# Optimization experiments

Hardware: AMD Instinct MI355X
Metric: run time of the kernel (lower is better)

The kernel has to match this reference:

```python
import jax, jax.numpy as jnp
import numpy as np

B, S, H = 64, 512, 768   # n_blocks, seq_len, hidden
C, M = 50, 2000          # n_characters, n_mentions
T = B * S                # total_seq_len
NEG_INF = -jnp.inf


def setup_inputs() -> dict:
    key = jax.random.key(0)
    ks = jax.random.split(key, 16)
    story_embeddings = jax.random.normal(ks[0], (B, S, H), dtype=jnp.float32)

    # additive log masks: 0.0 = allowed token, -inf = blocked (matches softmax(score + mask))
    names_bin = jax.random.bernoulli(ks[1], 0.05, (C, S)).at[:, 0].set(True)  # every char has >=1 name token
    names_mask = jnp.where(names_bin, 0.0, NEG_INF).astype(jnp.float32)

    utt_bin = jax.random.bernoulli(ks[2], 0.02, (C, T))
    utt_bin = utt_bin.at[40:].set(False)  # chars 40..49 have no utterances -> nan_to_num path
    utterances_mask = jnp.where(utt_bin, 0.0, NEG_INF).astype(jnp.float32)

    men_bin = jax.random.bernoulli(ks[3], 0.01, (M, T)).at[:, 0].set(True)
    mentions_mask = jnp.where(men_bin, 0.0, NEG_INF).astype(jnp.float32)

    mention_character_ids = jax.random.randint(ks[4], (M,), 0, 45, dtype=jnp.int32)  # chars 45..49 mention-less

    def lin(k):
        return 0.02 * jax.random.normal(k, (H,), dtype=jnp.float32)

    return {
        "story_embeddings": story_embeddings,
        "names_mask": names_mask,
        "utterances_mask": utterances_mask,
        "mentions_mask": mentions_mask,
        "mention_character_ids": mention_character_ids,
        "w_name_tok": lin(ks[5]), "b_name_tok": jnp.float32(0.0),
        "w_name": lin(ks[6]), "b_name": jnp.float32(0.0),
        "w_men_tok": lin(ks[7]), "b_men_tok": jnp.float32(0.0),
        "w_men": lin(ks[8]), "b_men": jnp.float32(0.0),
        "w_utt": lin(ks[9]), "b_utt": jnp.float32(0.0),
        "w_comb": lin(ks[10]), "b_comb": jnp.float32(0.0),
    }


def reference(story_embeddings, names_mask, utterances_mask, mentions_mask,
              mention_character_ids, w_name_tok, b_name_tok, w_name, b_name,
              w_men_tok, b_men_tok, w_men, b_men, w_utt, b_utt, w_comb, b_comb):
    n_char = names_mask.shape[0]
    n_blocks, seqlen, hidden = story_embeddings.shape
    se_flat = story_embeddings.reshape(n_blocks * seqlen, hidden)  # [T,H]

    # ---- name representation ----
    nts = story_embeddings @ w_name_tok + b_name_tok                       # [B,S]
    n_attn = jax.nn.softmax(nts[None, :, :] + names_mask[:, None, :], axis=2)  # [C,B,S]
    names_emb = jnp.einsum('cbs,bsh->cbh', n_attn, story_embeddings)       # [C,B,H]
    n_score = names_emb @ w_name + b_name                                  # [C,B]
    name_e = jnp.einsum('cb,cbh->ch', jax.nn.softmax(n_score, axis=1), names_emb)

    # ---- mention representation (segment softmax over mentions per character) ----
    mts = se_flat @ w_men_tok + b_men_tok                                  # [T]
    m_attn = jax.nn.softmax(mentions_mask + mts[None, :], axis=1)          # [M,T]
    m_emb = m_attn @ se_flat                                               # [M,H]
    m_score = m_emb @ w_men + b_men                                        # [M]
    seg = mention_character_ids
    seg_max = jax.ops.segment_max(m_score, seg, num_segments=n_char)       # [C]
    ex = jnp.exp(m_score - seg_max[seg])                                   # [M]
    den = jax.ops.segment_sum(ex, seg, num_segments=n_char)                # [C]
    mw = ex / den[seg]                                                     # [M]
    mention_e = jax.ops.segment_sum(mw[:, None] * m_emb, seg, num_segments=n_char)  # [C,H]; empty chars -> 0

    # ---- utterance representation ----
    uts = se_flat @ w_utt + b_utt                                          # [T]
    u_attn = jnp.nan_to_num(jax.nn.softmax(utterances_mask + uts[None, :], axis=1), nan=0.0)
    utt_e = u_attn @ se_flat                                               # [C,H]

    # ---- combine ----
    emb = jnp.stack([name_e, mention_e, utt_e], axis=1)                    # [C,3,H]
    score = emb @ w_comb + b_comb                                          # [C,3]
    has_mention = jax.ops.segment_sum(jnp.ones_like(m_score), seg, num_segments=n_char) > 0
    has_utt = jnp.any(utterances_mask == 0, axis=1)
    zeros = jnp.zeros((n_char,), dtype=score.dtype)
    mask = jnp.stack([zeros,
                      jnp.where(has_mention, 0.0, NEG_INF := -jnp.inf),
                      jnp.where(has_utt, 0.0, -jnp.inf)], axis=1)          # [C,3]
    attn = jax.nn.softmax(score + mask, axis=1)
    return jnp.einsum('ck,ckh->ch', attn, emb)                             # [C,H]
```

## Files before the change

### kernel.cpp

```cpp
#include <hip/hip_runtime.h>
#include <cmath>

#define Bn 64
#define Sn 512
#define Hn 768
#define Cn 50
#define Mn 2000
#define Tn (Bn*Sn)
#define MCAP 1024
#define NP 128
#define TC 256
#define HT 128

__global__ __launch_bounds__(256) void k_proj(
    const float* __restrict__ se,
    const float* __restrict__ w_ntok, const float* __restrict__ b_ntok,
    const float* __restrict__ w_name,
    const float* __restrict__ w_mtok, const float* __restrict__ b_mtok,
    const float* __restrict__ w_men,
    const float* __restrict__ w_utt, const float* __restrict__ b_utt,
    const float* __restrict__ w_comb,
    float* __restrict__ nts, float* __restrict__ p_name,
    float* __restrict__ mts, float* __restrict__ p_men,
    float* __restrict__ uts, float* __restrict__ p_comb)
{
    int wv = threadIdx.x >> 6, lane = threadIdx.x & 63;
    int gw = blockIdx.x * 4 + wv;
    float4 w[6][3];
    const float4* warr[6] = {(const float4*)w_ntok, (const float4*)w_name,
                             (const float4*)w_mtok, (const float4*)w_men,
                             (const float4*)w_utt,  (const float4*)w_comb};
#pragma unroll
    for (int j = 0; j < 6; j++)
#pragma unroll
        for (int k = 0; k < 3; k++) w[j][k] = warr[j][lane + 64*k];
    float b0 = b_ntok[0], b2 = b_mtok[0], b4 = b_utt[0];
    for (int rr = 0; rr < 8; rr++) {
        int r = gw*8 + rr;
        const float4* se4 = (const float4*)(se + (size_t)r * Hn);
        float s0=0,s1=0,s2=0,s3=0,s4=0,s5=0;
#pragma unroll
        for (int k = 0; k < 3; k++) {
            float4 v = se4[lane + 64*k];
            s0 += v.x*w[0][k].x + v.y*w[0][k].y + v.z*w[0][k].z + v.w*w[0][k].w;
            s1 += v.x*w[1][k].x + v.y*w[1][k].y + v.z*w[1][k].z + v.w*w[1][k].w;
            s2 += v.x*w[2][k].x + v.y*w[2][k].y + v.z*w[2][k].z + v.w*w[2][k].w;
            s3 += v.x*w[3][k].x + v.y*w[3][k].y + v.z*w[3][k].z + v.w*w[3][k].w;
            s4 += v.x*w[4][k].x + v.y*w[4][k].y + v.z*w[4][k].z + v.w*w[4][k].w;
            s5 += v.x*w[5][k].x + v.y*w[5][k].y + v.z*w[5][k].z + v.w*w[5][k].w;
        }
#pragma unroll
        for (int off = 32; off >= 1; off >>= 1) {
            s0 += __shfl_xor(s0, off); s1 += __shfl_xor(s1, off);
            s2 += __shfl_xor(s2, off); s3 += __shfl_xor(s3, off);
            s4 += __shfl_xor(s4, off); s5 += __shfl_xor(s5, off);
        }
        if (lane == 0) {
            nts[r]    = s0 + b0;
            p_name[r] = s1;
            mts[r]    = s2 + b2;
            p_men[r]  = s3;
            uts[r]    = s4 + b4;
            p_comb[r] = s5;
        }
    }
}

__global__ __launch_bounds__(256) void k_scan(
    const float* __restrict__ mmask, const float* __restrict__ mts,
    const float* __restrict__ p_men, const float* __restrict__ p_comb,
    const float* __restrict__ b_men_p,
    const float* __restrict__ umask, const float* __restrict__ uts,
    const float* __restrict__ nm_mask, const float* __restrict__ nts,
    const float* __restrict__ p_name, const float* __restrict__ b_name_p,
    float* __restrict__ m_score, float* __restrict__ mcv, float* __restrict__ denm,
    int* __restrict__ midx, float* __restrict__ mwgt, int* __restrict__ mcnt,
    float* __restrict__ m1u, float* __restrict__ denu, float* __restrict__ sc2,
    float* __restrict__ n_score, float* __restrict__ sc_n,
    float* __restrict__ m1n, float* __restrict__ denn)
{
    int tid = threadIdx.x;
    int wv = tid >> 6, lane = tid & 63;

    __shared__ int scnt;
    __shared__ int   sT[MCAP];
    __shared__ float sV[MCAP];
    __shared__ float sr1[4], sr2[4], sr3[4], sr4[4];

    if (blockIdx.x >= Mn + Cn) {
        int idx = (blockIdx.x - Mn - Cn) * 4 + wv;
        int c = idx >> 6, b = idx & 63;
        float v[8];
        float mx = -INFINITY;
#pragma unroll
        for (int k = 0; k < 8; k++) {
            int s = lane + 64*k;
            float val = nm_mask[c*Sn + s] + nts[b*Sn + s];
            v[k] = val;
            mx = fmaxf(mx, val);
        }
#pragma unroll
        for (int off = 32; off >= 1; off >>= 1) mx = fmaxf(mx, __shfl_xor(mx, off));
        float d = 0, sn = 0, sc = 0;
#pragma unroll
        for (int k = 0; k < 8; k++) {
            int s = lane + 64*k;
            int t = b*Sn + s;
            float e = __expf(v[k] - mx);
            d += e; sn += e * p_name[t]; sc += e * p_comb[t];
        }
#pragma unroll
        for (int off = 32; off >= 1; off >>= 1) {
            d += __shfl_xor(d, off); sn += __shfl_xor(sn, off); sc += __shfl_xor(sc, off);
        }
        if (lane == 0) {
            n_score[idx] = sn / d + b_name_p[0];
            sc_n[idx]    = sc / d;
            m1n[idx]     = mx;
            denn[idx]    = d;
        }
        return;
    }

    bool isU = blockIdx.x >= Mn;
    int row = isU ? (blockIdx.x - Mn) : blockIdx.x;
    if (tid == 0) scnt = 0;
    __syncthreads();

    const float4* row4 = (const float4*)((isU ? umask : mmask) + (size_t)row * Tn);
    const float*  vals = isU ? uts : mts;

    for (int k = 0; k < Tn/4/256; k++) {
        int i = tid + k*256;
        float4 f = row4[i];
        float fm[4] = {f.x, f.y, f.z, f.w};
#pragma unroll
        for (int j = 0; j < 4; j++) {
            bool act = (fm[j] == 0.0f);
            unsigned long long bm = __ballot(act);
            if (bm) {
                int tot = __popcll(bm);
                int pos = __popcll(bm & ((1ull << lane) - 1ull));
                int base;
                if (lane == 0) base = atomicAdd(&scnt, tot);
                base = __builtin_amdgcn_readfirstlane(base);
                int s = base + pos;
                if (act && s < MCAP) sT[s] = i*4 + j;
            }
        }
    }
    __syncthreads();
    int n = (scnt < MCAP) ? scnt : MCAP;

    float mx = -INFINITY;
    for (int i = tid; i < n; i += 256) {
        float v = vals[sT[i]];
        sV[i] = v;
        mx = fmaxf(mx, v);
    }
#pragma unroll
    for (int off = 32; off >= 1; off >>= 1) mx = fmaxf(mx, __shfl_xor(mx, off));
    if (lane == 0) sr1[wv] = mx;
    __syncthreads();
    mx = fmaxf(fmaxf(sr1[0], sr1[1]), fmaxf(sr1[2], sr1[3]));

    float d = 0, nm = 0, nc = 0;
    if (!isU) {
        int* gi = midx + (size_t)row * MCAP;
        float* gwp = mwgt + (size_t)row * MCAP;
        for (int i = tid; i < n; i += 256) {
            float e = __expf(sV[i] - mx);
            int t = sT[i];
            d += e; nm += e * p_men[t]; nc += e * p_comb[t];
            gi[i] = t; gwp[i] = e;
        }
    } else {
        for (int i = tid; i < n; i += 256) {
            float e = __expf(sV[i] - mx);
            d += e; nc += e * p_comb[sT[i]];
        }
    }
#pragma unroll
    for (int off = 32; off >= 1; off >>= 1) {
        d += __shfl_xor(d, off); nm += __shfl_xor(nm, off); nc += __shfl_xor(nc, off);
    }
    if (lane == 0) { sr2[wv] = d; sr3[wv] = nm; sr4[wv] = nc; }
    __syncthreads();
    if (tid == 0) {
        float dd = sr2[0]+sr2[1]+sr2[2]+sr2[3];
        float sm = sr3[0]+sr3[1]+sr3[2]+sr3[3];
        float sc = sr4[0]+sr4[1]+sr4[2]+sr4[3];
        if (!isU) {
            m_score[row] = sm/dd + b_men_p[0];
            mcv[row]     = sc/dd;
            denm[row]    = dd;
            mcnt[row]    = n;
        } else {
            m1u[row]  = mx;
            denu[row] = dd;
            sc2[row]  = (dd > 0.f) ? sc/dd : 0.f;
        }
    }
}

__global__ __launch_bounds__(256) void k_small(
    const float* __restrict__ n_score, const float* __restrict__ sc_n,
    const int* __restrict__ seg, const float* __restrict__ m_score, const float* __restrict__ mcv,
    float* __restrict__ bw, float* __restrict__ sc0,
    float* __restrict__ segmax, float* __restrict__ segden, float* __restrict__ sc1)
{
    int tid = threadIdx.x;
    if (blockIdx.x < Cn) {
        int c = blockIdx.x;
        if (tid < 64) {
            int lane = tid;
            int idx = c*Bn + lane;
            float v = n_score[idx];
            float mx = v;
#pragma unroll
            for (int off = 32; off >= 1; off >>= 1) mx = fmaxf(mx, __shfl_xor(mx, off));
            float e = __expf(v - mx);
            float d = e, s = e * sc_n[idx];
#pragma unroll
            for (int off = 32; off >= 1; off >>= 1) { d += __shfl_xor(d, off); s += __shfl_xor(s, off); }
            bw[idx] = e / d;
            if (lane == 0) sc0[c] = s / d;
        }
    } else {
        int c = blockIdx.x - Cn;
        float mx = -INFINITY;
        for (int m = tid; m < Mn; m += 256)
            if (seg[m] == c) mx = fmaxf(mx, m_score[m]);
        __shared__ float sm[256];
        sm[tid] = mx; __syncthreads();
        for (int s = 128; s > 0; s >>= 1) { if (tid < s) sm[tid] = fmaxf(sm[tid], sm[tid+s]); __syncthreads(); }
        mx = sm[0];
        float d = 0, s1 = 0;
        if (mx != -INFINITY) {
            for (int m = tid; m < Mn; m += 256)
                if (seg[m] == c) { float e = __expf(m_score[m] - mx); d += e; s1 += e * mcv[m]; }
        }
        __shared__ float sd[256], ss[256];
        sd[tid] = d; ss[tid] = s1; __syncthreads();
        for (int s = 128; s > 0; s >>= 1) { if (tid < s) { sd[tid] += sd[tid+s]; ss[tid] += ss[tid+s]; } __syncthreads(); }
        if (tid == 0) {
            segmax[c] = mx;
            segden[c] = sd[0];
            sc1[c]    = (sd[0] > 0.f) ? ss[0]/sd[0] : 0.f;
        }
    }
}

__device__ inline void combine_attn(float sc0v, float sc1v, float sc2v,
                                    float sdn, float dnu, float bc,
                                    float& a0, float& a1, float& a2)
{
    float s0 = sc0v + bc;
    bool hasm = sdn > 0.f, hasu = dnu > 0.f;
    float s1 = hasm ? sc1v + bc : -INFINITY;
    float s2 = hasu ? sc2v + bc : -INFINITY;
    float mx = fmaxf(s0, fmaxf(s1, s2));
    float e0 = __expf(s0 - mx);
    float e1 = hasm ? __expf(s1 - mx) : 0.f;
    float e2 = hasu ? __expf(s2 - mx) : 0.f;
    float dd = e0 + e1 + e2;
    a0 = e0/dd; a1 = e1/dd; a2 = e2/dd;
}

__global__ __launch_bounds__(256) void k_buildW(
    const float* __restrict__ nm_mask, const float* __restrict__ nts,
    const float* __restrict__ m1n, const float* __restrict__ denn,
    const float* __restrict__ bw,
    const float* __restrict__ umask, const float* __restrict__ uts,
    const float* __restrict__ m1u, const float* __restrict__ denu,
    const float* __restrict__ sc0, const float* __restrict__ sc1, const float* __restrict__ sc2,
    const float* __restrict__ segden, const float* __restrict__ b_comb_p,
    float* __restrict__ W)
{
    int c = blockIdx.y;
    float a0, a1, a2;
    combine_attn(sc0[c], sc1[c], sc2[c], segden[c], denu[c], b_comb_p[0], a0, a1, a2);
    int t0 = (blockIdx.x * 256 + threadIdx.x) * 4;
    int b = t0 >> 9;
    float4 um = *(const float4*)(umask + (size_t)c * Tn + t0);
    float cn = a0 * bw[c*Bn + b] / denn[c*Bn + b];
    float m1nc = m1n[c*Bn + b];
    float du = denu[c];
    float cu = (du > 0.f) ? a2 / du : 0.f;
    float m1uc = m1u[c];
    float umj[4] = {um.x, um.y, um.z, um.w};
    float rj[4];
#pragma unroll
    for (int j = 0; j < 4; j++) {
        int t = t0 + j;
        int s = t & (Sn-1);
        float w = 0.f;
        if (nm_mask[c*Sn + s] == 0.f) w += cn * __expf(nts[t] - m1nc);
        if (umj[j] == 0.f)            w += cu * __expf(uts[t] - m1uc);
        rj[j] = w;
    }
    *(float4*)(W + (size_t)c * Tn + t0) = make_float4(rj[0], rj[1], rj[2], rj[3]);
}

__global__ __launch_bounds__(64) void k_scatter_men(
    const int* __restrict__ midx, const float* __restrict__ mwgt, const int* __restrict__ mcnt,
    const int* __restrict__ seg,
    const float* __restrict__ m_score, const float* __restrict__ denm,
    const float* __restrict__ segmax, const float* __restrict__ segden,
    const float* __restrict__ sc0, const float* __restrict__ sc1, const float* __restrict__ sc2,
    const float* __restrict__ denu, const float* __restrict__ b_comb_p,
    float* __restrict__ W)
{
    int m = blockIdx.x, tid = threadIdx.x;
    int c = seg[m];
    float a0, a1, a2;
    combine_attn(sc0[c], sc1[c], sc2[c], segden[c], denu[c], b_comb_p[0], a0, a1, a2);
    float coef = a1 * __expf(m_score[m] - segmax[c]) / segden[c] / denm[m];
    int n = mcnt[m];
    const int* gi = midx + (size_t)m * MCAP;
    const float* gwp = mwgt + (size_t)m * MCAP;
    float* Wc = W + (size_t)c * Tn;
    for (int i = tid; i < n; i += 64)
        atomicAdd(&Wc[gi[i]], coef * gwp[i]);
}

#define FMA4(A, WS, V) { A.x += (WS)*(V).x; A.y += (WS)*(V).y; A.z += (WS)*(V).z; A.w += (WS)*(V).w; }
__global__ __launch_bounds__(256) void k_out1(
    const float* __restrict__ W, const float* __restrict__ se, float* __restrict__ partial)
{
    int p = blockIdx.x;
    int h0 = blockIdx.y * HT;
    int tid = threadIdx.x;
    int x = tid & 31, y = tid >> 5;
    __shared__ float sW[56][64];
    __shared__ float sS[64][128];
    float4 acc[7];
#pragma unroll
    for (int i = 0; i < 7; i++) acc[i] = make_float4(0,0,0,0);
    for (int sub = 0; sub < 4; sub++) {
        int tbase = p*TC + sub*64;
        for (int i = tid; i < 896; i += 256) {
            int c = i >> 4, f = i & 15;
            float4 v = (c < Cn) ? *(const float4*)(W + (size_t)c * Tn + tbase + f*4)
                                : make_float4(0,0,0,0);
            *(float4*)&sW[c][f*4] = v;
        }
#pragma unroll
        for (int q = 0; q < 8; q++) {
            int idx = tid + q*256;
            int row = idx >> 5, col = idx & 31;
            *(float4*)&sS[row][col*4] =
                *(const float4*)(se + (size_t)(tbase + row) * Hn + h0 + col*4);
        }
        __syncthreads();
        for (int t4 = 0; t4 < 64; t4 += 4) {
            float4 wq[7];
#pragma unroll
            for (int cc = 0; cc < 7; cc++)
                wq[cc] = *(const float4*)&sW[y*7 + cc][t4];
            float4 v0 = *(const float4*)&sS[t4+0][x*4];
            float4 v1 = *(const float4*)&sS[t4+1][x*4];
            float4 v2 = *(const float4*)&sS[t4+2][x*4];
            float4 v3 = *(const float4*)&sS[t4+3][x*4];
#pragma unroll
            for (int cc = 0; cc < 7; cc++) {
                FMA4(acc[cc], wq[cc].x, v0);
                FMA4(acc[cc], wq[cc].y, v1);
                FMA4(acc[cc], wq[cc].z, v2);
                FMA4(acc[cc], wq[cc].w, v3);
            }
        }
        __syncthreads();
    }
#pragma unroll
    for (int cc = 0; cc < 7; cc++) {
        int c = y*7 + cc;
        if (c < Cn)
            *(float4*)(partial + ((size_t)p * Cn + c) * Hn + h0 + x*4) = acc[cc];
    }
}

__global__ __launch_bounds__(256) void k_out2(
    const float* __restrict__ partial, float* __restrict__ out)
{
    int cell = blockIdx.x * 256 + threadIdx.x;
    if (cell < Cn*Hn) {
        float s = 0.f;
#pragma unroll 8
        for (int p = 0; p < NP; p++)
            s += partial[(size_t)p * (Cn*Hn) + cell];
        out[cell] = s;
    }
}

extern "C" void kernel_launch(void* const* d_in, const int* in_sizes, int n_in,
                              void* d_out, int out_size, void* d_ws, size_t ws_size,
                              hipStream_t stream) {
    const float* se      = (const float*)d_in[0];
    const float* nm_mask = (const float*)d_in[1];
    const float* umask   = (const float*)d_in[2];
    const float* mmask   = (const float*)d_in[3];
    const int*   seg     = (const int*)  d_in[4];
    const float* w_ntok  = (const float*)d_in[5];
    const float* b_ntok  = (const float*)d_in[6];
    const float* w_name  = (const float*)d_in[7];
    const float* b_name  = (const float*)d_in[8];
    const float* w_mtok  = (const float*)d_in[9];
    const float* b_mtok  = (const float*)d_in[10];
    const float* w_men   = (const float*)d_in[11];
    const float* b_men   = (const float*)d_in[12];
    const float* w_utt   = (const float*)d_in[13];
    const float* b_utt   = (const float*)d_in[14];
    const float* w_comb  = (const float*)d_in[15];
    const float* b_comb  = (const float*)d_in[16];
    float* out = (float*)d_out;

    float* ws = (float*)d_ws;
    float* partial = ws;
    float* W       = partial + (size_t)NP*Cn*Hn;
    float* nts     = W + (size_t)Cn*Tn;
    float* p_name  = nts + Tn;
    float* mts     = p_name + Tn;
    float* p_men   = mts + Tn;
    float* uts     = p_men + Tn;
    float* p_comb  = uts + Tn;
    float* n_score = p_comb + Tn;
    float* sc_n    = n_score + Cn*Bn;
    float* bw      = sc_n + Cn*Bn;
    float* m1n     = bw + Cn*Bn;
    float* denn    = m1n + Cn*Bn;
    float* m_score = denn + Cn*Bn;
    float* mcv     = m_score + Mn;
    float* denm    = mcv + Mn;
    float* mwgt    = denm + Mn;
    int*   midx    = (int*)(mwgt + (size_t)Mn*MCAP);
    int*   mcnt    = midx + (size_t)Mn*MCAP;
    float* segmax  = (float*)(mcnt + Mn);
    float* segden  = segmax + Cn;
    float* sc0     = segden + Cn;
    float* sc1     = sc0 + Cn;
    float* sc2     = sc1 + Cn;
    float* m1u     = sc2 + Cn;
    float* denu    = m1u + Cn;

    k_proj<<<1024, 256, 0, stream>>>(se, w_ntok, b_ntok, w_name, w_mtok, b_mtok,
                                     w_men, w_utt, b_utt, w_comb,
                                     nts, p_name, mts, p_men, uts, p_comb);

    k_scan<<<Mn + Cn + (Cn*Bn)/4, 256, 0, stream>>>(
        mmask, mts, p_men, p_comb, b_men,
        umask, uts,
        nm_mask, nts, p_name, b_name,
        m_score, mcv, denm, midx, mwgt, mcnt,
        m1u, denu, sc2,
        n_score, sc_n, m1n, denn);

    k_small<<<2*Cn, 256, 0, stream>>>(n_score, sc_n, seg, m_score, mcv,
                                      bw, sc0, segmax, segden, sc1);

    k_buildW<<<dim3(Tn/1024, Cn), 256, 0, stream>>>(nm_mask, nts, m1n, denn, bw,
                                                    umask, uts, m1u, denu,
                                                    sc0, sc1, sc2, segden, b_comb, W);

    k_scatter_men<<<Mn, 64, 0, stream>>>(midx, mwgt, mcnt, seg, m_score, denm,
                                         segmax, segden, sc0, sc1, sc2, denu, b_comb, W);

    k_out1<<<dim3(NP, Hn/HT), 256, 0, stream>>>(W, se, partial);
    k_out2<<<(Cn*Hn + 255)/256, 256, 0, stream>>>(partial, out);
}
```

Before: 188.4 us.

## Overlap mask scanning with projection and scatter utterance weights sparsely

Merges the projection kernel with the mask-index scan into one launch. Projection blocks are interleaved with scan blocks so the memory-bound mask scan no longer waits for the projection to finish. The index lists now go to global memory, and a second kernel computes the softmax weights from them. The utterance contribution to W is moved out of the dense buildW pass, which re-read the 50x32768 utterance mask, and into the sparse atomic scatter kernel. The cost is extra global traffic for the index lists and more atomics on W.

New measurement: 205.7 us. 9.2% more time.

```diff
diff --git a/kernel.cpp b/kernel.cpp
--- a/kernel.cpp
+++ b/kernel.cpp
@@ -11,9 +11,10 @@
 #define NP 128
 #define TC 256
 #define HT 128
-
-__global__ __launch_bounds__(256) void k_proj(
-    const float* __restrict__ se,
+#define NR (Mn + Cn)
+
+__global__ __launch_bounds__(256) void k_A(
+    const float* __restrict__ se, const float* __restrict__ mmask, const float* __restrict__ umask,
     const float* __restrict__ w_ntok, const float* __restrict__ b_ntok,
     const float* __restrict__ w_name,
     const float* __restrict__ w_mtok, const float* __restrict__ b_mtok,
@@ -22,114 +23,68 @@
     const float* __restrict__ w_comb,
     float* __restrict__ nts, float* __restrict__ p_name,
     float* __restrict__ mts, float* __restrict__ p_men,
-    float* __restrict__ uts, float* __restrict__ p_comb)
-{
-    int wv = threadIdx.x >> 6, lane = threadIdx.x & 63;
-    int gw = blockIdx.x * 4 + wv;
-    float4 w[6][3];
-    const float4* warr[6] = {(const float4*)w_ntok, (const float4*)w_name,
-                             (const float4*)w_mtok, (const float4*)w_men,
-                             (const float4*)w_utt,  (const float4*)w_comb};
-#pragma unroll
-    for (int j = 0; j < 6; j++)
-#pragma unroll
-        for (int k = 0; k < 3; k++) w[j][k] = warr[j][lane + 64*k];
-    float b0 = b_ntok[0], b2 = b_mtok[0], b4 = b_utt[0];
-    for (int rr = 0; rr < 8; rr++) {
-        int r = gw*8 + rr;
-        const float4* se4 = (const float4*)(se + (size_t)r * Hn);
-        float s0=0,s1=0,s2=0,s3=0,s4=0,s5=0;
-#pragma unroll
-        for (int k = 0; k < 3; k++) {
-            float4 v = se4[lane + 64*k];
-            s0 += v.x*w[0][k].x + v.y*w[0][k].y + v.z*w[0][k].z + v.w*w[0][k].w;
-            s1 += v.x*w[1][k].x + v.y*w[1][k].y + v.z*w[1][k].z + v.w*w[1][k].w;
-            s2 += v.x*w[2][k].x + v.y*w[2][k].y + v.z*w[2][k].z + v.w*w[2][k].w;
-            s3 += v.x*w[3][k].x + v.y*w[3][k].y + v.z*w[3][k].z + v.w*w[3][k].w;
-            s4 += v.x*w[4][k].x + v.y*w[4][k].y + v.z*w[4][k].z + v.w*w[4][k].w;
-            s5 += v.x*w[5][k].x + v.y*w[5][k].y + v.z*w[5][k].z + v.w*w[5][k].w;
-        }
-#pragma unroll
-        for (int off = 32; off >= 1; off >>= 1) {
-            s0 += __shfl_xor(s0, off); s1 += __shfl_xor(s1, off);
-            s2 += __shfl_xor(s2, off); s3 += __shfl_xor(s3, off);
-            s4 += __shfl_xor(s4, off); s5 += __shfl_xor(s5, off);
-        }
-        if (lane == 0) {
-            nts[r]    = s0 + b0;
-            p_name[r] = s1;
-            mts[r]    = s2 + b2;
-            p_men[r]  = s3;
-            uts[r]    = s4 + b4;
-            p_comb[r] = s5;
-        }
-    }
-}
-
-__global__ __launch_bounds__(256) void k_scan(
-    const float* __restrict__ mmask, const float* __restrict__ mts,
-    const float* __restrict__ p_men, const float* __restrict__ p_comb,
-    const float* __restrict__ b_men_p,
-    const float* __restrict__ umask, const float* __restrict__ uts,
-    const float* __restrict__ nm_mask, const float* __restrict__ nts,
-    const float* __restrict__ p_name, const float* __restrict__ b_name_p,
-    float* __restrict__ m_score, float* __restrict__ mcv, float* __restrict__ denm,
-    int* __restrict__ midx, float* __restrict__ mwgt, int* __restrict__ mcnt,
-    float* __restrict__ m1u, float* __restrict__ denu, float* __restrict__ sc2,
-    float* __restrict__ n_score, float* __restrict__ sc_n,
-    float* __restrict__ m1n, float* __restrict__ denn)
-{
-    int tid = threadIdx.x;
-    int wv = tid >> 6, lane = tid & 63;
-
+    float* __restrict__ uts, float* __restrict__ p_comb,
+    int* __restrict__ midx, int* __restrict__ mcnt,
+    int* __restrict__ uidx, int* __restrict__ ucnt)
+{
+    int bid = blockIdx.x;
+    int tid = threadIdx.x, wv = tid >> 6, lane = tid & 63;
+
+    int cid = -1, pb = -1;
+    if (bid >= 3072)            cid = 2048 + (bid - 3072);
+    else if (bid % 3 == 2)      pb  = bid / 3;
+    else                        cid = (bid / 3) * 2 + (bid % 3);
+
+    if (pb >= 0) {
+        int gw = pb * 4 + wv;
+        float4 w[6][3];
+        const float4* warr[6] = {(const float4*)w_ntok, (const float4*)w_name,
+                                 (const float4*)w_mtok, (const float4*)w_men,
+                                 (const float4*)w_utt,  (const float4*)w_comb};
+#pragma unroll
+        for (int j = 0; j < 6; j++)
+#pragma unroll
+            for (int k = 0; k < 3; k++) w[j][k] = warr[j][lane + 64*k];
+        float b0 = b_ntok[0], b2 = b_mtok[0], b4 = b_utt[0];
+        for (int rr = 0; rr < 8; rr++) {
+            int r = gw*8 + rr;
+            const float4* se4 = (const float4*)(se + (size_t)r * Hn);
+            float s0=0,s1=0,s2=0,s3=0,s4=0,s5=0;
+#pragma unroll
+            for (int k = 0; k < 3; k++) {
+                float4 v = se4[lane + 64*k];
+                s0 += v.x*w[0][k].x + v.y*w[0][k].y + v.z*w[0][k].z + v.w*w[0][k].w;
+                s1 += v.x*w[1][k].x + v.y*w[1][k].y + v.z*w[1][k].z + v.w*w[1][k].w;
+                s2 += v.x*w[2][k].x + v.y*w[2][k].y + v.z*w[2][k].z + v.w*w[2][k].w;
+                s3 += v.x*w[3][k].x + v.y*w[3][k].y + v.z*w[3][k].z + v.w*w[3][k].w;
+                s4 += v.x*w[4][k].x + v.y*w[4][k].y + v.z*w[4][k].z + v.w*w[4][k].w;
+                s5 += v.x*w[5][k].x + v.y*w[5][k].y + v.z*w[5][k].z + v.w*w[5][k].w;
+            }
+#pragma unroll
+            for (int off = 32; off >= 1; off >>= 1) {
+                s0 += __shfl_xor(s0, off); s1 += __shfl_xor(s1, off);
+                s2 += __shfl_xor(s2, off); s3 += __shfl_xor(s3, off);
+                s4 += __shfl_xor(s4, off); s5 += __shfl_xor(s5, off);
+            }
+            if (lane == 0) {
+                nts[r]    = s0 + b0;
+                p_name[r] = s1;
+                mts[r]    = s2 + b2;
+                p_men[r]  = s3;
+                uts[r]    = s4 + b4;
+                p_comb[r] = s5;
+            }
+        }
+        return;
+    }
+
+    bool isU = cid >= Mn;
+    int row = isU ? (cid - Mn) : cid;
+    const float4* row4 = (const float4*)((isU ? umask : mmask) + (size_t)row * Tn);
+    int* list = isU ? (uidx + (size_t)row * MCAP) : (midx + (size_t)row * MCAP);
     __shared__ int scnt;
-    __shared__ int   sT[MCAP];
-    __shared__ float sV[MCAP];
-    __shared__ float sr1[4], sr2[4], sr3[4], sr4[4];
-
-    if (blockIdx.x >= Mn + Cn) {
-        int idx = (blockIdx.x - Mn - Cn) * 4 + wv;
-        int c = idx >> 6, b = idx & 63;
-        float v[8];
-        float mx = -INFINITY;
-#pragma unroll
-        for (int k = 0; k < 8; k++) {
-            int s = lane + 64*k;
-            float val = nm_mask[c*Sn + s] + nts[b*Sn + s];
-            v[k] = val;
-            mx = fmaxf(mx, val);
-        }
-#pragma unroll
-        for (int off = 32; off >= 1; off >>= 1) mx = fmaxf(mx, __shfl_xor(mx, off));
-        float d = 0, sn = 0, sc = 0;
-#pragma unroll
-        for (int k = 0; k < 8; k++) {
-            int s = lane + 64*k;
-            int t = b*Sn + s;
-            float e = __expf(v[k] - mx);
-            d += e; sn += e * p_name[t]; sc += e * p_comb[t];
-        }
-#pragma unroll
-        for (int off = 32; off >= 1; off >>= 1) {
-            d += __shfl_xor(d, off); sn += __shfl_xor(sn, off); sc += __shfl_xor(sc, off);
-        }
-        if (lane == 0) {
-            n_score[idx] = sn / d + b_name_p[0];
-            sc_n[idx]    = sc / d;
-            m1n[idx]     = mx;
-            denn[idx]    = d;
-        }
-        return;
-    }
-
-    bool isU = blockIdx.x >= Mn;
-    int row = isU ? (blockIdx.x - Mn) : blockIdx.x;
     if (tid == 0) scnt = 0;
     __syncthreads();
-
-    const float4* row4 = (const float4*)((isU ? umask : mmask) + (size_t)row * Tn);
-    const float*  vals = isU ? uts : mts;
-
     for (int k = 0; k < Tn/4/256; k++) {
         int i = tid + k*256;
         float4 f = row4[i];
@@ -141,20 +96,85 @@
             if (bm) {
                 int tot = __popcll(bm);
                 int pos = __popcll(bm & ((1ull << lane) - 1ull));
-                int base;
+                int base = 0;
                 if (lane == 0) base = atomicAdd(&scnt, tot);
                 base = __builtin_amdgcn_readfirstlane(base);
                 int s = base + pos;
-                if (act && s < MCAP) sT[s] = i*4 + j;
+                if (act && s < MCAP) list[s] = i*4 + j;
             }
         }
     }
     __syncthreads();
-    int n = (scnt < MCAP) ? scnt : MCAP;
+    if (tid == 0) {
+        int n = (scnt < MCAP) ? scnt : MCAP;
+        if (isU) ucnt[row] = n; else mcnt[row] = n;
+    }
+}
+
+__global__ __launch_bounds__(256) void k_B(
+    const float* __restrict__ mts, const float* __restrict__ uts,
+    const float* __restrict__ p_men, const float* __restrict__ p_comb,
+    const float* __restrict__ p_name,
+    const float* __restrict__ b_men_p, const float* __restrict__ b_name_p,
+    const float* __restrict__ nm_mask, const float* __restrict__ nts,
+    const int* __restrict__ midx, const int* __restrict__ mcnt,
+    const int* __restrict__ uidx, const int* __restrict__ ucnt,
+    float* __restrict__ m_score, float* __restrict__ mcv, float* __restrict__ denm,
+    float* __restrict__ mwgt,
+    float* __restrict__ denu, float* __restrict__ sc2, float* __restrict__ uwgt,
+    float* __restrict__ n_score, float* __restrict__ sc_n,
+    float* __restrict__ m1n, float* __restrict__ denn)
+{
+    int bid = blockIdx.x;
+    int tid = threadIdx.x, wv = tid >> 6, lane = tid & 63;
+
+    if (bid >= NR) {
+        int idx = (bid - NR) * 4 + wv;
+        int c = idx >> 6, b = idx & 63;
+        float v[8];
+        float mx = -INFINITY;
+#pragma unroll
+        for (int k = 0; k < 8; k++) {
+            int s = lane + 64*k;
+            float val = nm_mask[c*Sn + s] + nts[b*Sn + s];
+            v[k] = val;
+            mx = fmaxf(mx, val);
+        }
+#pragma unroll
+        for (int off = 32; off >= 1; off >>= 1) mx = fmaxf(mx, __shfl_xor(mx, off));
+        float d = 0, sn = 0, sc = 0;
+#pragma unroll
+        for (int k = 0; k < 8; k++) {
+            int s = lane + 64*k;
+            int t = b*Sn + s;
+            float e = __expf(v[k] - mx);
+            d += e; sn += e * p_name[t]; sc += e * p_comb[t];
+        }
+#pragma unroll
+        for (int off = 32; off >= 1; off >>= 1) {
+            d += __shfl_xor(d, off); sn += __shfl_xor(sn, off); sc += __shfl_xor(sc, off);
+        }
+        if (lane == 0) {
+            n_score[idx] = sn / d + b_name_p[0];
+            sc_n[idx]    = sc / d;
+            m1n[idx]     = mx;
+            denn[idx]    = d;
+        }
+        return;
+    }
+
+    bool isU = bid >= Mn;
+    int row = isU ? (bid - Mn) : bid;
+    int n = isU ? ucnt[row] : mcnt[row];
+    const int* gi = isU ? (uidx + (size_t)row * MCAP) : (midx + (size_t)row * MCAP);
+    const float* vals = isU ? uts : mts;
+
+    __shared__ float sV[MCAP];
+    __shared__ float sr1[4], sr2[4], sr3[4], sr4[4];
 
     float mx = -INFINITY;
     for (int i = tid; i < n; i += 256) {
-        float v = vals[sT[i]];
+        float v = vals[gi[i]];
         sV[i] = v;
         mx = fmaxf(mx, v);
     }
@@ -165,20 +185,13 @@
     mx = fmaxf(fmaxf(sr1[0], sr1[1]), fmaxf(sr1[2], sr1[3]));
 
     float d = 0, nm = 0, nc = 0;
-    if (!isU) {
-        int* gi = midx + (size_t)row * MCAP;
-        float* gwp = mwgt + (size_t)row * MCAP;
-        for (int i = tid; i < n; i += 256) {
-            float e = __expf(sV[i] - mx);
-            int t = sT[i];
-            d += e; nm += e * p_men[t]; nc += e * p_comb[t];
-            gi[i] = t; gwp[i] = e;
-        }
-    } else {
-        for (int i = tid; i < n; i += 256) {
-            float e = __expf(sV[i] - mx);
-            d += e; nc += e * p_comb[sT[i]];
-        }
+    float* wout = isU ? (uwgt + (size_t)row * MCAP) : (mwgt + (size_t)row * MCAP);
+    for (int i = tid; i < n; i += 256) {
+        float e = __expf(sV[i] - mx);
+        int t = gi[i];
+        d += e; nc += e * p_comb[t];
+        if (!isU) nm += e * p_men[t];
+        wout[i] = e;
     }
 #pragma unroll
     for (int off = 32; off >= 1; off >>= 1) {
@@ -194,9 +207,7 @@
             m_score[row] = sm/dd + b_men_p[0];
             mcv[row]     = sc/dd;
             denm[row]    = dd;
-            mcnt[row]    = n;
         } else {
-            m1u[row]  = mx;
             denu[row] = dd;
             sc2[row]  = (dd > 0.f) ? sc/dd : 0.f;
         }
@@ -271,8 +282,7 @@
     const float* __restrict__ nm_mask, const float* __restrict__ nts,
     const float* __restrict__ m1n, const float* __restrict__ denn,
     const float* __restrict__ bw,
-    const float* __restrict__ umask, const float* __restrict__ uts,
-    const float* __restrict__ m1u, const float* __restrict__ denu,
+    const float* __restrict__ denu,
     const float* __restrict__ sc0, const float* __restrict__ sc1, const float* __restrict__ sc2,
     const float* __restrict__ segden, const float* __restrict__ b_comb_p,
     float* __restrict__ W)
@@ -282,28 +292,21 @@
     combine_attn(sc0[c], sc1[c], sc2[c], segden[c], denu[c], b_comb_p[0], a0, a1, a2);
     int t0 = (blockIdx.x * 256 + threadIdx.x) * 4;
     int b = t0 >> 9;
-    float4 um = *(const float4*)(umask + (size_t)c * Tn + t0);
     float cn = a0 * bw[c*Bn + b] / denn[c*Bn + b];
     float m1nc = m1n[c*Bn + b];
-    float du = denu[c];
-    float cu = (du > 0.f) ? a2 / du : 0.f;
-    float m1uc = m1u[c];
-    float umj[4] = {um.x, um.y, um.z, um.w};
     float rj[4];
 #pragma unroll
     for (int j = 0; j < 4; j++) {
         int t = t0 + j;
         int s = t & (Sn-1);
-        float w = 0.f;
-        if (nm_mask[c*Sn + s] == 0.f) w += cn * __expf(nts[t] - m1nc);
-        if (umj[j] == 0.f)            w += cu * __expf(uts[t] - m1uc);
-        rj[j] = w;
+        rj[j] = (nm_mask[c*Sn + s] == 0.f) ? cn * __expf(nts[t] - m1nc) : 0.f;
     }
     *(float4*)(W + (size_t)c * Tn + t0) = make_float4(rj[0], rj[1], rj[2], rj[3]);
 }
 
-__global__ __launch_bounds__(64) void k_scatter_men(
+__global__ __launch_bounds__(64) void k_scatter(
     const int* __restrict__ midx, const float* __restrict__ mwgt, const int* __restrict__ mcnt,
+    const int* __restrict__ uidx, const float* __restrict__ uwgt, const int* __restrict__ ucnt,
     const int* __restrict__ seg,
     const float* __restrict__ m_score, const float* __restrict__ denm,
     const float* __restrict__ segmax, const float* __restrict__ segden,
@@ -311,17 +314,33 @@
     const float* __restrict__ denu, const float* __restrict__ b_comb_p,
     float* __restrict__ W)
 {
-    int m = blockIdx.x, tid = threadIdx.x;
-    int c = seg[m];
-    float a0, a1, a2;
-    combine_attn(sc0[c], sc1[c], sc2[c], segden[c], denu[c], b_comb_p[0], a0, a1, a2);
-    float coef = a1 * __expf(m_score[m] - segmax[c]) / segden[c] / denm[m];
-    int n = mcnt[m];
-    const int* gi = midx + (size_t)m * MCAP;
-    const float* gwp = mwgt + (size_t)m * MCAP;
-    float* Wc = W + (size_t)c * Tn;
-    for (int i = tid; i < n; i += 64)
-        atomicAdd(&Wc[gi[i]], coef * gwp[i]);
+    int bid = blockIdx.x, tid = threadIdx.x;
+    if (bid < Mn) {
+        int m = bid;
+        int c = seg[m];
+        float a0, a1, a2;
+        combine_attn(sc0[c], sc1[c], sc2[c], segden[c], denu[c], b_comb_p[0], a0, a1, a2);
+        float coef = a1 * __expf(m_score[m] - segmax[c]) / segden[c] / denm[m];
+        int n = mcnt[m];
+        const int* gi = midx + (size_t)m * MCAP;
+        const float* gwp = mwgt + (size_t)m * MCAP;
+        float* Wc = W + (size_t)c * Tn;
+        for (int i = tid; i < n; i += 64)
+            atomicAdd(&Wc[gi[i]], coef * gwp[i]);
+    } else {
+        int c = bid - Mn;
+        float dn = denu[c];
+        if (dn <= 0.f) return;
+        float a0, a1, a2;
+        combine_attn(sc0[c], sc1[c], sc2[c], segden[c], dn, b_comb_p[0], a0, a1, a2);
+        float coef = a2 / dn;
+        int n = ucnt[c];
+        const int* gi = uidx + (size_t)c * MCAP;
+        const float* gwp = uwgt + (size_t)c * MCAP;
+        float* Wc = W + (size_t)c * Tn;
+        for (int i = tid; i < n; i += 64)
+            atomicAdd(&Wc[gi[i]], coef * gwp[i]);
+    }
 }
 
 #define FMA4(A, WS, V) { A.x += (WS)*(V).x; A.y += (WS)*(V).y; A.z += (WS)*(V).z; A.w += (WS)*(V).w; }
@@ -435,35 +454,38 @@
     float* mwgt    = denm + Mn;
     int*   midx    = (int*)(mwgt + (size_t)Mn*MCAP);
     int*   mcnt    = midx + (size_t)Mn*MCAP;
-    float* segmax  = (float*)(mcnt + Mn);
+    float* uwgt    = (float*)(mcnt + Mn);
+    int*   uidx    = (int*)(uwgt + (size_t)Cn*MCAP);
+    int*   ucnt    = uidx + (size_t)Cn*MCAP;
+    float* segmax  = (float*)(ucnt + Cn);
     float* segden  = segmax + Cn;
     float* sc0     = segden + Cn;
     float* sc1     = sc0 + Cn;
     float* sc2     = sc1 + Cn;
-    float* m1u     = sc2 + Cn;
-    float* denu    = m1u + Cn;
-
-    k_proj<<<1024, 256, 0, stream>>>(se, w_ntok, b_ntok, w_name, w_mtok, b_mtok,
-                                     w_men, w_utt, b_utt, w_comb,
-                                     nts, p_name, mts, p_men, uts, p_comb);
-
-    k_scan<<<Mn + Cn + (Cn*Bn)/4, 256, 0, stream>>>(
-        mmask, mts, p_men, p_comb, b_men,
-        umask, uts,
-        nm_mask, nts, p_name, b_name,
-        m_score, mcv, denm, midx, mwgt, mcnt,
-        m1u, denu, sc2,
-        n_score, sc_n, m1n, denn);
+    float* denu    = sc2 + Cn;
+
+    k_A<<<3074, 256, 0, stream>>>(se, mmask, umask,
+                                  w_ntok, b_ntok, w_name, w_mtok, b_mtok,
+                                  w_men, w_utt, b_utt, w_comb,
+                                  nts, p_name, mts, p_men, uts, p_comb,
+                                  midx, mcnt, uidx, ucnt);
+
+    k_B<<<NR + (Cn*Bn)/4, 256, 0, stream>>>(mts, uts, p_men, p_comb, p_name,
+                                            b_men, b_name, nm_mask, nts,
+                                            midx, mcnt, uidx, ucnt,
+                                            m_score, mcv, denm, mwgt,
+                                            denu, sc2, uwgt,
+                                            n_score, sc_n, m1n, denn);
 
     k_small<<<2*Cn, 256, 0, stream>>>(n_score, sc_n, seg, m_score, mcv,
                                       bw, sc0, segmax, segden, sc1);
 
     k_buildW<<<dim3(Tn/1024, Cn), 256, 0, stream>>>(nm_mask, nts, m1n, denn, bw,
-                                                    umask, uts, m1u, denu,
-                                                    sc0, sc1, sc2, segden, b_comb, W);
-
-    k_scatter_men<<<Mn, 64, 0, stream>>>(midx, mwgt, mcnt, seg, m_score, denm,
-                                         segmax, segden, sc0, sc1, sc2, denu, b_comb, W);
+                                                    denu, sc0, sc1, sc2, segden, b_comb, W);
+
+    k_scatter<<<Mn + Cn, 64, 0, stream>>>(midx, mwgt, mcnt, uidx, uwgt, ucnt,
+                                          seg, m_score, denm, segmax, segden,
+                                          sc0, sc1, sc2, denu, b_comb, W);
 
     k_out1<<<dim3(NP, Hn/HT), 256, 0, stream>>>(W, se, partial);
     k_out2<<<(Cn*Hn + 255)/256, 256, 0, stream>>>(partial, out);
```
